# Kernel tuning notes

Measured on AMD Instinct MI355X. Metric: run time of the kernel, lower is better.

Reference implementation:

```python
import jax, jax.numpy as jnp
import numpy as np

IN_FEATURES = 4096
OUT_FEATURES = 11008
GROUPSIZE = 128
Q_MAX = 127  # 8-bit activation quant


def setup_inputs() -> dict:
    key = jax.random.key(0)
    k1, k2, k3, k4, k5 = jax.random.split(key, 5)
    x = jax.random.normal(k1, (4, 2048, IN_FEATURES), dtype=jnp.float32)
    # packed int4 weights: two nibbles per byte, stored as int32 byte values
    qweight = jax.random.randint(k2, (OUT_FEATURES * IN_FEATURES // 2,), 0, 256, dtype=jnp.int32)
    n_groups = OUT_FEATURES * IN_FEATURES // GROUPSIZE
    wscales = jax.random.uniform(k3, (n_groups, 1), dtype=jnp.float32) * 0.01 + 1e-4
    wzeros = jax.random.randint(k4, (n_groups, 1), 0, 16, dtype=jnp.int32)
    bias = jax.random.normal(k5, (OUT_FEATURES,), dtype=jnp.float32)
    return {"x": x, "qweight": qweight, "wscales": wscales, "wzeros": wzeros, "bias": bias}


def _act_quant_per_token(t):
    # t: [tokens, in_features]; per-token absmax symmetric 8-bit fake quant
    scales = jnp.maximum(jnp.max(jnp.abs(t), axis=-1, keepdims=True), 1e-5) / Q_MAX
    return jnp.clip(jnp.round(t / scales), -Q_MAX - 1, Q_MAX) * scales


def _unpack_weight(qweight, wscales, wzeros):
    # python_decompress: hi nibble then lo nibble, each in [0,16)
    hi = (qweight >> 4) & 15
    lo = qweight & 15
    fint = jnp.stack([hi, lo], axis=-1).reshape(-1, GROUPSIZE).astype(jnp.float32)
    w = (fint - wzeros.astype(jnp.float32)) * wscales  # [n_groups, groupsize]
    return w.reshape(OUT_FEATURES, IN_FEATURES)


def reference(x, qweight, wscales, wzeros, bias):
    out_shape = x.shape[:-1] + (OUT_FEATURES,)
    t = x.reshape(-1, x.shape[-1])
    t = _act_quant_per_token(t)
    w = _unpack_weight(qweight, wscales, wzeros)
    out = t @ w.T + bias
    return out.reshape(out_shape)
```

## Files before the change

kernel.cpp:

```cpp
#include <hip/hip_runtime.h>
#include <stdint.h>


#define IN_F 4096
#define OUT_F 11008
#define GS 128

#define BM 128
#define BN 128
#define BK 128
#define NKT (IN_F / BK)

using i32x4 = __attribute__((ext_vector_type(4))) int;
using f32x4 = __attribute__((ext_vector_type(4))) float;

__global__ __launch_bounds__(256) void act_quant_kernel(
    const float* __restrict__ x, int8_t* __restrict__ q, float* __restrict__ sc) {
  __shared__ float wmax[4];
  const int tok = blockIdx.x;
  const int tid = threadIdx.x;
  const float* xr = x + (size_t)tok * IN_F + tid * 16;

  f32x4 v[4];
  float am = 0.f;
#pragma unroll
  for (int i = 0; i < 4; ++i) {
    v[i] = *(const f32x4*)(xr + i * 4);
#pragma unroll
    for (int j = 0; j < 4; ++j) am = fmaxf(am, fabsf(v[i][j]));
  }
#pragma unroll
  for (int off = 1; off < 64; off <<= 1) am = fmaxf(am, __shfl_xor(am, off));
  if ((tid & 63) == 0) wmax[tid >> 6] = am;
  __syncthreads();
  am = fmaxf(fmaxf(wmax[0], wmax[1]), fmaxf(wmax[2], wmax[3]));
  const float scale = fmaxf(am, 1e-5f) / 127.0f;

  i32x4 pk;
#pragma unroll
  for (int i = 0; i < 4; ++i) {
    uint32_t w = 0;
#pragma unroll
    for (int j = 0; j < 4; ++j) {
      float r = rintf(v[i][j] / scale);
      r = fminf(fmaxf(r, -128.f), 127.f);
      int iv = (int)r;
      w |= (uint32_t)(iv & 255) << (8 * j);
    }
    pk[i] = (int)w;
  }
  *(i32x4*)(q + (size_t)tok * IN_F + tid * 16) = pk;
  if (tid == 0) sc[tok] = scale;
}

__global__ __launch_bounds__(256) void unpack_kernel(
    const int* __restrict__ qw, const int* __restrict__ wz, int8_t* __restrict__ w8) {
  const int t = blockIdx.x * 256 + threadIdx.x;
  const int z = wz[t >> 3];
  const i32x4 a = *(const i32x4*)(qw + (size_t)t * 8);
  const i32x4 b = *(const i32x4*)(qw + (size_t)t * 8 + 4);
  int vals[8];
#pragma unroll
  for (int i = 0; i < 4; ++i) { vals[i] = a[i]; vals[4 + i] = b[i]; }
  i32x4 outw;
#pragma unroll
  for (int h = 0; h < 4; ++h) {
    const int x0 = vals[2 * h], x1 = vals[2 * h + 1];
    const int w0 = ((x0 >> 4) & 15) - z;
    const int w1 = (x0 & 15) - z;
    const int w2 = ((x1 >> 4) & 15) - z;
    const int w3 = (x1 & 15) - z;
    outw[h] = (w0 & 255) | ((w1 & 255) << 8) | ((w2 & 255) << 16) | ((w3 & 255) << 24);
  }
  *(i32x4*)(w8 + (size_t)t * 16) = outw;
}

__global__ __launch_bounds__(256) void gemm_kernel(
    const int8_t* __restrict__ Aq, const int8_t* __restrict__ Bq,
    const float* __restrict__ asc, const float* __restrict__ wsc,
    const float* __restrict__ bias, float* __restrict__ out) {
  __shared__ int8_t As[BM * BK];
  __shared__ int8_t Bs[BN * BK];
  __shared__ float Ws[NKT * BN];

  const int tid = threadIdx.x;
  const int lane = tid & 63;
  const int wid = tid >> 6;
  const int bm0 = blockIdx.y * BM;
  const int bn0 = blockIdx.x * BN;
  const int wm = (wid >> 1) * 64;
  const int wn = (wid & 1) * 64;

  {
    const float* src = wsc + (size_t)bn0 * NKT;
    const int u0 = tid * 16;
    const int col = u0 >> 5;
    const int g0 = u0 & 31;
    f32x4 t0 = *(const f32x4*)(src + u0);
    f32x4 t1 = *(const f32x4*)(src + u0 + 4);
    f32x4 t2 = *(const f32x4*)(src + u0 + 8);
    f32x4 t3 = *(const f32x4*)(src + u0 + 12);
#pragma unroll
    for (int j = 0; j < 4; ++j) {
      Ws[(g0 + j) * BN + col] = t0[j];
      Ws[(g0 + 4 + j) * BN + col] = t1[j];
      Ws[(g0 + 8 + j) * BN + col] = t2[j];
      Ws[(g0 + 12 + j) * BN + col] = t3[j];
    }
  }

  f32x4 facc[4][4] = {};

  const int8_t* Abase = Aq + (size_t)bm0 * IN_F;
  const int8_t* Bbase = Bq + (size_t)bn0 * IN_F;
  const int srow = tid >> 3;
  const int kbp = (tid & 7) << 4;

  for (int kt = 0; kt < NKT; ++kt) {
    __syncthreads();
#pragma unroll
    for (int p = 0; p < 4; ++p) {
      const int row = p * 32 + srow;
      const int kb = kbp ^ ((row & 7) << 4);
      __builtin_amdgcn_global_load_lds(
          (const __attribute__((address_space(1))) void*)(Abase + (size_t)row * IN_F + kt * BK + kb),
          (__attribute__((address_space(3))) void*)(As + p * 4096 + wid * 1024), 16, 0, 0);
    }
#pragma unroll
    for (int p = 0; p < 4; ++p) {
      const int row = p * 32 + srow;
      const int kb = kbp ^ ((row & 7) << 4);
      __builtin_amdgcn_global_load_lds(
          (const __attribute__((address_space(1))) void*)(Bbase + (size_t)row * IN_F + kt * BK + kb),
          (__attribute__((address_space(3))) void*)(Bs + p * 4096 + wid * 1024), 16, 0, 0);
    }
    __syncthreads();

    i32x4 iacc[4][4] = {};
#pragma unroll
    for (int kk = 0; kk < 2; ++kk) {
      const int s = kk * 64 + (lane >> 4) * 16;
      i32x4 af[4], bf[4];
#pragma unroll
      for (int i = 0; i < 4; ++i) {
        const int r = wm + i * 16 + (lane & 15);
        af[i] = *(const i32x4*)(As + r * BK + (s ^ ((r & 7) << 4)));
      }
#pragma unroll
      for (int j = 0; j < 4; ++j) {
        const int c = wn + j * 16 + (lane & 15);
        bf[j] = *(const i32x4*)(Bs + c * BK + (s ^ ((c & 7) << 4)));
      }
#pragma unroll
      for (int i = 0; i < 4; ++i)
#pragma unroll
        for (int j = 0; j < 4; ++j)
          iacc[i][j] = __builtin_amdgcn_mfma_i32_16x16x64_i8(af[i], bf[j], iacc[i][j], 0, 0, 0);
    }

#pragma unroll
    for (int j = 0; j < 4; ++j) {
      const float wsj = Ws[kt * BN + wn + j * 16 + (lane & 15)];
#pragma unroll
      for (int i = 0; i < 4; ++i)
#pragma unroll
        for (int e = 0; e < 4; ++e)
          facc[i][j][e] += wsj * (float)iacc[i][j][e];
    }
  }

  const int r0 = (lane >> 4) * 4;
  const int cl = lane & 15;
#pragma unroll
  for (int i = 0; i < 4; ++i) {
#pragma unroll
    for (int e = 0; e < 4; ++e) {
      const int m = bm0 + wm + i * 16 + r0 + e;
      const float a = asc[m];
      float* orow = out + (size_t)m * OUT_F + bn0 + wn;
#pragma unroll
      for (int j = 0; j < 4; ++j) {
        const int n = j * 16 + cl;
        orow[n] = facc[i][j][e] * a + bias[bn0 + wn + n];
      }
    }
  }
}

extern "C" void kernel_launch(void* const* d_in, const int* in_sizes, int n_in,
                              void* d_out, int out_size, void* d_ws, size_t ws_size,
                              hipStream_t stream) {
  const float* x = (const float*)d_in[0];
  const int* qw = (const int*)d_in[1];
  const float* wsc = (const float*)d_in[2];
  const int* wz = (const int*)d_in[3];
  const float* bias = (const float*)d_in[4];
  float* out = (float*)d_out;

  const int tokens = in_sizes[0] / IN_F;

  int8_t* w8 = (int8_t*)d_ws;
  int8_t* q8 = w8 + (size_t)OUT_F * IN_F;
  float* sc = (float*)(q8 + (size_t)tokens * IN_F);

  act_quant_kernel<<<tokens, 256, 0, stream>>>(x, q8, sc);
  unpack_kernel<<<(OUT_F * IN_F / 2 / 8) / 256, 256, 0, stream>>>(qw, wz, w8);
  gemm_kernel<<<dim3(OUT_F / BN, tokens / BM), 256, 0, stream>>>(q8, w8, sc, wsc, bias, out);
}
```

Before: 1.058 ms.

## Restructure int8 GEMM with 256x256 tiles, 4-buffer LDS pipeline and fp16 scales

The GEMM moves to 256x256 output tiles with 512 threads and BK=64. It keeps a four-slot LDS ring that issues global-to-LDS loads two steps ahead, interleaved with the MFMA phases, and synchronises with explicit vmcnt waits and barriers. It also adds a block-index swizzle for L2 locality, stores group scales as fp16 in LDS, and applies the scale after every non-accumulating MFMA. The activation-quant and unpack kernels change their access patterns to coalesced 4-byte and 8-byte per-thread chunks. The goals are more data reuse per tile and hiding memory latency. In exchange the float rescale work per MFMA doubles, LDS use becomes very high, and fp16 scales lose a little precision.

After: 1.311 ms. +24.0%, slower.

```diff
diff --git a/kernel.cpp b/kernel.cpp
--- a/kernel.cpp
+++ b/kernel.cpp
@@ -4,13 +4,15 @@
 
 #define IN_F 4096
 #define OUT_F 11008
-#define GS 128
-
-#define BM 128
-#define BN 128
-#define BK 128
-#define NKT (IN_F / BK)
-
+
+#define BM 256
+#define BN 256
+#define BK 64
+#define NT (IN_F / BK)
+#define NG 32
+#define BUFSZ (BM * BK)
+
+using i32x2 = __attribute__((ext_vector_type(2))) int;
 using i32x4 = __attribute__((ext_vector_type(4))) int;
 using f32x4 = __attribute__((ext_vector_type(4))) float;
 
@@ -19,13 +21,13 @@
   __shared__ float wmax[4];
   const int tok = blockIdx.x;
   const int tid = threadIdx.x;
-  const float* xr = x + (size_t)tok * IN_F + tid * 16;
+  const float* xr = x + (size_t)tok * IN_F;
 
   f32x4 v[4];
   float am = 0.f;
 #pragma unroll
   for (int i = 0; i < 4; ++i) {
-    v[i] = *(const f32x4*)(xr + i * 4);
+    v[i] = *(const f32x4*)(xr + i * 1024 + tid * 4);
 #pragma unroll
     for (int j = 0; j < 4; ++j) am = fmaxf(am, fabsf(v[i][j]));
   }
@@ -36,7 +38,6 @@
   am = fmaxf(fmaxf(wmax[0], wmax[1]), fmaxf(wmax[2], wmax[3]));
   const float scale = fmaxf(am, 1e-5f) / 127.0f;
 
-  i32x4 pk;
 #pragma unroll
   for (int i = 0; i < 4; ++i) {
     uint32_t w = 0;
@@ -47,144 +48,143 @@
       int iv = (int)r;
       w |= (uint32_t)(iv & 255) << (8 * j);
     }
-    pk[i] = (int)w;
-  }
-  *(i32x4*)(q + (size_t)tok * IN_F + tid * 16) = pk;
+    *(uint32_t*)(q + (size_t)tok * IN_F + i * 1024 + tid * 4) = w;
+  }
   if (tid == 0) sc[tok] = scale;
 }
 
 __global__ __launch_bounds__(256) void unpack_kernel(
     const int* __restrict__ qw, const int* __restrict__ wz, int8_t* __restrict__ w8) {
   const int t = blockIdx.x * 256 + threadIdx.x;
-  const int z = wz[t >> 3];
-  const i32x4 a = *(const i32x4*)(qw + (size_t)t * 8);
-  const i32x4 b = *(const i32x4*)(qw + (size_t)t * 8 + 4);
-  int vals[8];
-#pragma unroll
-  for (int i = 0; i < 4; ++i) { vals[i] = a[i]; vals[4 + i] = b[i]; }
-  i32x4 outw;
-#pragma unroll
-  for (int h = 0; h < 4; ++h) {
-    const int x0 = vals[2 * h], x1 = vals[2 * h + 1];
+  const int z = wz[t >> 4];
+  const i32x4 a = *(const i32x4*)(qw + (size_t)t * 4);
+  i32x2 o;
+#pragma unroll
+  for (int h = 0; h < 2; ++h) {
+    const int x0 = a[2 * h], x1 = a[2 * h + 1];
     const int w0 = ((x0 >> 4) & 15) - z;
     const int w1 = (x0 & 15) - z;
     const int w2 = ((x1 >> 4) & 15) - z;
     const int w3 = (x1 & 15) - z;
-    outw[h] = (w0 & 255) | ((w1 & 255) << 8) | ((w2 & 255) << 16) | ((w3 & 255) << 24);
-  }
-  *(i32x4*)(w8 + (size_t)t * 16) = outw;
-}
-
-__global__ __launch_bounds__(256) void gemm_kernel(
+    o[h] = (w0 & 255) | ((w1 & 255) << 8) | ((w2 & 255) << 16) | ((w3 & 255) << 24);
+  }
+  *(i32x2*)(w8 + (size_t)t * 8) = o;
+}
+
+__global__ __launch_bounds__(512, 2) void gemm_kernel(
     const int8_t* __restrict__ Aq, const int8_t* __restrict__ Bq,
     const float* __restrict__ asc, const float* __restrict__ wsc,
     const float* __restrict__ bias, float* __restrict__ out) {
-  __shared__ int8_t As[BM * BK];
-  __shared__ int8_t Bs[BN * BK];
-  __shared__ float Ws[NKT * BN];
+  __shared__ int8_t As_l[4 * BUFSZ];
+  __shared__ int8_t Bs_l[4 * BUFSZ];
+  __shared__ _Float16 Wsh[NG * BN];
 
   const int tid = threadIdx.x;
   const int lane = tid & 63;
   const int wid = tid >> 6;
-  const int bm0 = blockIdx.y * BM;
-  const int bn0 = blockIdx.x * BN;
-  const int wm = (wid >> 1) * 64;
-  const int wn = (wid & 1) * 64;
-
-  {
-    const float* src = wsc + (size_t)bn0 * NKT;
-    const int u0 = tid * 16;
-    const int col = u0 >> 5;
-    const int g0 = u0 & 31;
-    f32x4 t0 = *(const f32x4*)(src + u0);
-    f32x4 t1 = *(const f32x4*)(src + u0 + 4);
-    f32x4 t2 = *(const f32x4*)(src + u0 + 8);
-    f32x4 t3 = *(const f32x4*)(src + u0 + 12);
-#pragma unroll
-    for (int j = 0; j < 4; ++j) {
-      Ws[(g0 + j) * BN + col] = t0[j];
-      Ws[(g0 + 4 + j) * BN + col] = t1[j];
-      Ws[(g0 + 8 + j) * BN + col] = t2[j];
-      Ws[(g0 + 12 + j) * BN + col] = t3[j];
-    }
-  }
-
-  f32x4 facc[4][4] = {};
+
+  const int bid = blockIdx.x;
+  const int swz = (bid & 7) * 172 + (bid >> 3);
+  const int bm0 = (swz / 43) * BM;
+  const int bn0 = (swz % 43) * BN;
+
+  const int wm = (wid >> 2) * 128;
+  const int wn = (wid & 3) * 64;
+  const int cl = lane & 15;
+  const int ksw = ((lane >> 4) ^ ((cl >> 1) & 3)) * 16;
+  const int regA = (wm + cl) * BK + ksw;
+  const int regB = (wn + cl) * BK + ksw;
 
   const int8_t* Abase = Aq + (size_t)bm0 * IN_F;
   const int8_t* Bbase = Bq + (size_t)bn0 * IN_F;
-  const int srow = tid >> 3;
-  const int kbp = (tid & 7) << 4;
-
-  for (int kt = 0; kt < NKT; ++kt) {
-    __syncthreads();
-#pragma unroll
-    for (int p = 0; p < 4; ++p) {
-      const int row = p * 32 + srow;
-      const int kb = kbp ^ ((row & 7) << 4);
-      __builtin_amdgcn_global_load_lds(
-          (const __attribute__((address_space(1))) void*)(Abase + (size_t)row * IN_F + kt * BK + kb),
-          (__attribute__((address_space(3))) void*)(As + p * 4096 + wid * 1024), 16, 0, 0);
+
+  {
+    const int c = tid >> 1, g0 = (tid & 1) * 16;
+    const float* src = wsc + (size_t)(bn0 + c) * NG + g0;
+#pragma unroll
+    for (int k = 0; k < 16; k += 4) {
+      f32x4 v = *(const f32x4*)(src + k);
+#pragma unroll
+      for (int e = 0; e < 4; ++e) Wsh[(g0 + k + e) * BN + c] = (_Float16)v[e];
     }
-#pragma unroll
-    for (int p = 0; p < 4; ++p) {
-      const int row = p * 32 + srow;
-      const int kb = kbp ^ ((row & 7) << 4);
-      __builtin_amdgcn_global_load_lds(
-          (const __attribute__((address_space(1))) void*)(Bbase + (size_t)row * IN_F + kt * BK + kb),
-          (__attribute__((address_space(3))) void*)(Bs + p * 4096 + wid * 1024), 16, 0, 0);
+  }
+
+#define STAGE(gbase, st, h, lbuf) do {                                         \
+    const int _row = (h) * 128 + (tid >> 2);                                   \
+    const int _ck = (tid & 3) ^ ((tid >> 3) & 3);                              \
+    __builtin_amdgcn_global_load_lds(                                          \
+      (const __attribute__((address_space(1))) void*)(                         \
+          (gbase) + (size_t)_row * IN_F + (st) * BK + _ck * 16),               \
+      (__attribute__((address_space(3))) void*)(                               \
+          (lbuf) + (h) * 8192 + wid * 1024), 16, 0, 0);                        \
+  } while (0)
+
+  STAGE(Abase, 0, 0, As_l); STAGE(Abase, 0, 1, As_l);
+  STAGE(Bbase, 0, 0, Bs_l); STAGE(Bbase, 0, 1, Bs_l);
+  STAGE(Abase, 1, 0, As_l + BUFSZ); STAGE(Abase, 1, 1, As_l + BUFSZ);
+  STAGE(Bbase, 1, 0, Bs_l + BUFSZ); STAGE(Bbase, 1, 1, Bs_l + BUFSZ);
+  __syncthreads();
+
+  f32x4 facc[8][4] = {};
+  const i32x4 izero = {0, 0, 0, 0};
+
+#define PHASE(QM, QN, STAGE_STMT) do {                                         \
+    STAGE_STMT;                                                                \
+    i32x4 af[4], bf[2];                                                        \
+    _Float16 wh0 = Wsh[g * BN + wn + ((QN) * 2 + 0) * 16 + cl];                \
+    _Float16 wh1 = Wsh[g * BN + wn + ((QN) * 2 + 1) * 16 + cl];                \
+    _Pragma("unroll")                                                          \
+    for (int i = 0; i < 4; ++i)                                                \
+      af[i] = *(const i32x4*)(ab + regA + ((QM) * 4 + i) * 1024);              \
+    bf[0] = *(const i32x4*)(bb + regB + ((QN) * 2 + 0) * 1024);                \
+    bf[1] = *(const i32x4*)(bb + regB + ((QN) * 2 + 1) * 1024);                \
+    __builtin_amdgcn_s_setprio(1);                                             \
+    const float w0 = (float)wh0, w1 = (float)wh1;                              \
+    _Pragma("unroll")                                                          \
+    for (int i = 0; i < 4; ++i) {                                              \
+      i32x4 t0 = __builtin_amdgcn_mfma_i32_16x16x64_i8(af[i], bf[0], izero, 0, 0, 0); \
+      i32x4 t1 = __builtin_amdgcn_mfma_i32_16x16x64_i8(af[i], bf[1], izero, 0, 0, 0); \
+      _Pragma("unroll")                                                        \
+      for (int e = 0; e < 4; ++e) {                                            \
+        facc[(QM) * 4 + i][(QN) * 2 + 0][e] += w0 * (float)t0[e];              \
+        facc[(QM) * 4 + i][(QN) * 2 + 1][e] += w1 * (float)t1[e];              \
+      }                                                                        \
+    }                                                                          \
+    __builtin_amdgcn_s_setprio(0);                                             \
+  } while (0)
+
+  for (int t = 0; t < NT; ++t) {
+    const int8_t* ab = As_l + (t & 3) * BUFSZ;
+    const int8_t* bb = Bs_l + (t & 3) * BUFSZ;
+    int8_t* sa = As_l + ((t + 2) & 3) * BUFSZ;
+    int8_t* sb = Bs_l + ((t + 2) & 3) * BUFSZ;
+    const int g = t >> 1;
+    const bool dost = (t + 2) < NT;
+
+    PHASE(0, 0, if (dost) STAGE(Abase, t + 2, 0, sa));
+    PHASE(0, 1, if (dost) STAGE(Abase, t + 2, 1, sa));
+    PHASE(1, 0, if (dost) STAGE(Bbase, t + 2, 0, sb));
+    PHASE(1, 1, if (dost) STAGE(Bbase, t + 2, 1, sb));
+
+    asm volatile("s_waitcnt vmcnt(4)" ::: "memory");
+    __builtin_amdgcn_s_barrier();
+  }
+
+  const int r0 = (lane >> 4) * 4;
+#pragma unroll
+  for (int i = 0; i < 8; ++i) {
+    const int mrow = bm0 + wm + i * 16 + r0;
+    f32x4 a4 = *(const f32x4*)(asc + mrow);
+#pragma unroll
+    for (int e = 0; e < 4; ++e) {
+      float* orow = out + (size_t)(mrow + e) * OUT_F + bn0 + wn + cl;
+#pragma unroll
+      for (int j = 0; j < 4; ++j)
+        orow[j * 16] = facc[i][j][e] * a4[e] + bias[bn0 + wn + j * 16 + cl];
     }
-    __syncthreads();
-
-    i32x4 iacc[4][4] = {};
-#pragma unroll
-    for (int kk = 0; kk < 2; ++kk) {
-      const int s = kk * 64 + (lane >> 4) * 16;
-      i32x4 af[4], bf[4];
-#pragma unroll
-      for (int i = 0; i < 4; ++i) {
-        const int r = wm + i * 16 + (lane & 15);
-        af[i] = *(const i32x4*)(As + r * BK + (s ^ ((r & 7) << 4)));
-      }
-#pragma unroll
-      for (int j = 0; j < 4; ++j) {
-        const int c = wn + j * 16 + (lane & 15);
-        bf[j] = *(const i32x4*)(Bs + c * BK + (s ^ ((c & 7) << 4)));
-      }
-#pragma unroll
-      for (int i = 0; i < 4; ++i)
-#pragma unroll
-        for (int j = 0; j < 4; ++j)
-          iacc[i][j] = __builtin_amdgcn_mfma_i32_16x16x64_i8(af[i], bf[j], iacc[i][j], 0, 0, 0);
-    }
-
-#pragma unroll
-    for (int j = 0; j < 4; ++j) {
-      const float wsj = Ws[kt * BN + wn + j * 16 + (lane & 15)];
-#pragma unroll
-      for (int i = 0; i < 4; ++i)
-#pragma unroll
-        for (int e = 0; e < 4; ++e)
-          facc[i][j][e] += wsj * (float)iacc[i][j][e];
-    }
-  }
-
-  const int r0 = (lane >> 4) * 4;
-  const int cl = lane & 15;
-#pragma unroll
-  for (int i = 0; i < 4; ++i) {
-#pragma unroll
-    for (int e = 0; e < 4; ++e) {
-      const int m = bm0 + wm + i * 16 + r0 + e;
-      const float a = asc[m];
-      float* orow = out + (size_t)m * OUT_F + bn0 + wn;
-#pragma unroll
-      for (int j = 0; j < 4; ++j) {
-        const int n = j * 16 + cl;
-        orow[n] = facc[i][j][e] * a + bias[bn0 + wn + n];
-      }
-    }
-  }
+  }
+#undef PHASE
+#undef STAGE
 }
 
 extern "C" void kernel_launch(void* const* d_in, const int* in_sizes, int n_in,
@@ -204,6 +204,6 @@
   float* sc = (float*)(q8 + (size_t)tokens * IN_F);
 
   act_quant_kernel<<<tokens, 256, 0, stream>>>(x, q8, sc);
-  unpack_kernel<<<(OUT_F * IN_F / 2 / 8) / 256, 256, 0, stream>>>(qw, wz, w8);
-  gemm_kernel<<<dim3(OUT_F / BN, tokens / BM), 256, 0, stream>>>(q8, w8, sc, wsc, bias, out);
-}
+  unpack_kernel<<<(OUT_F * IN_F / 2 / 4) / 256, 256, 0, stream>>>(qw, wz, w8);
+  gemm_kernel<<<(tokens / BM) * (OUT_F / BN), 512, 0, stream>>>(q8, w8, sc, wsc, bias, out);
+}
```
